# Kernel tuning notes

Hardware: AMD Instinct MI355X
Metric: run time of the kernel (lower is better)

## Reference

```python
import jax, jax.numpy as jnp
import numpy as np

MARGIN = 0.2


def _pairwise_euclidean(x):
    # [B, D] -> [B, B] euclidean distance matrix (safe sqrt: zero grad at d=0,
    # matching torch.cdist subgradient; diagonal is never used by the loss).
    sq = jnp.sum(x * x, axis=1)
    d2 = sq[:, None] + sq[None, :] - 2.0 * (x @ x.T)
    d2 = jnp.maximum(d2, 0.0)
    safe = jnp.where(d2 > 0, d2, 1.0)
    return jnp.where(d2 > 0, jnp.sqrt(safe), 0.0)


def setup_inputs() -> dict:
    key = jax.random.key(0)
    k1, k2 = jax.random.split(key)
    B, D = 256, 768
    return {
        "img_tokens": jax.random.normal(k1, (B, D), dtype=jnp.float32),
        "ehr_tokens": jax.random.normal(k2, (B, D), dtype=jnp.float32),
    }


def reference(img_tokens, ehr_tokens):
    B = img_tokens.shape[0]
    d_ehr = _pairwise_euclidean(ehr_tokens)  # [B, B]
    d_img = _pairwise_euclidean(img_tokens)  # [B, B]

    # Broadcast to [i, j, k] triplet grids.
    e_ij = d_ehr[:, :, None]
    e_ik = d_ehr[:, None, :]
    g_ij = d_img[:, :, None]
    g_ik = d_img[:, None, :]

    loss = jnp.where(
        e_ij < e_ik,
        jax.nn.relu(g_ij - g_ik + MARGIN),
        jnp.where(
            e_ik < e_ij,
            jax.nn.relu(g_ik - g_ij + MARGIN),
            jnp.abs(g_ij - g_ik),
        ),
    )  # [B, B, B]

    i = jnp.arange(B)[:, None, None]
    j = jnp.arange(B)[None, :, None]
    k = jnp.arange(B)[None, None, :]
    mask = (j < k) & (i != j) & (i != k)  # valid triplets: i!=j, i!=k, j<k

    num_triplets = B * (B - 1) * (B - 2) // 2  # B * C(B-1, 2)
    total = jnp.sum(jnp.where(mask, loss, 0.0))
    return total / num_triplets
```

## Files before the change

### kernel.cpp

```cpp
#include <hip/hip_runtime.h>
#include <math.h>

#define NB 256
#define ND 768
#define MARGIN_F 0.2f
#define NKC 16
#define KCF 48
#define PITCH 64

__global__ __launch_bounds__(256)
void dist_kernel(const float* __restrict__ Ximg,
                 const float* __restrict__ Xehr,
                 float* __restrict__ planes) {
    __shared__ float As[64 * PITCH];
    __shared__ float Bs[64 * PITCH];

    const int tid = threadIdx.x;
    const int bid = blockIdx.x;

    const int m    = bid >> 8;
    const int r    = bid & 255;
    const int tile = r >> 4;
    const int kc   = r & 15;
    const int ti   = tile >> 2;
    const int tj   = tile & 3;
    const float* __restrict__ X = m ? Xehr : Ximg;
    const int base_col = kc * KCF;

#pragma unroll
    for (int p = 0; p < 3; ++p) {
        const int idx = tid + (p << 8);
        const int row = idx / 12;
        const int c4  = idx - row * 12;
        const int sw  = (row >> 2) & 7;
        const float4 va = *(const float4*)(&X[(size_t)(ti * 64 + row) * ND + base_col + c4 * 4]);
        *(float4*)(&As[row * PITCH + ((c4 ^ sw) << 2)]) = va;
        const float4 vb = *(const float4*)(&X[(size_t)(tj * 64 + row) * ND + base_col + c4 * 4]);
        *(float4*)(&Bs[row * PITCH + ((c4 ^ sw) << 2)]) = vb;
    }
    __syncthreads();

    const int li = tid >> 4;
    const int lj = tid & 15;
    const int swa = li & 7;
    const int swb = lj & 7;

    float acc[4][4];
#pragma unroll
    for (int a = 0; a < 4; ++a)
#pragma unroll
        for (int b = 0; b < 4; ++b) acc[a][b] = 0.0f;

#pragma unroll 4
    for (int q = 0; q < 12; ++q) {
        float4 av[4], bv[4];
#pragma unroll
        for (int a = 0; a < 4; ++a)
            av[a] = *(const float4*)(&As[(4 * li + a) * PITCH + ((q ^ swa) << 2)]);
#pragma unroll
        for (int b = 0; b < 4; ++b)
            bv[b] = *(const float4*)(&Bs[(4 * lj + b) * PITCH + ((q ^ swb) << 2)]);
#pragma unroll
        for (int a = 0; a < 4; ++a)
#pragma unroll
            for (int b = 0; b < 4; ++b) {
                const float d0 = av[a].x - bv[b].x;
                const float d1 = av[a].y - bv[b].y;
                const float d2 = av[a].z - bv[b].z;
                const float d3 = av[a].w - bv[b].w;
                acc[a][b] += d0 * d0 + d1 * d1 + d2 * d2 + d3 * d3;
            }
    }

    float* P = planes + (((size_t)m * NKC + kc) << 16);
#pragma unroll
    for (int a = 0; a < 4; ++a) {
        const int gi = ti * 64 + 4 * li + a;
        float4 v;
        v.x = acc[a][0]; v.y = acc[a][1]; v.z = acc[a][2]; v.w = acc[a][3];
        *(float4*)(&P[(size_t)gi * NB + tj * 64 + 4 * lj]) = v;
    }
}

__global__ __launch_bounds__(512)
void triplet_kernel(const float* __restrict__ planes,
                    float* __restrict__ partials) {
    __shared__ float Es[NB], Gs[NB];
    __shared__ float pg[2][NB], pe[2][NB];
    __shared__ float wred[8];

    const int tid = threadIdx.x;
    const int i   = blockIdx.x;
    const int k   = tid & 255;
    const int h   = tid >> 8;

    float sg = 0.0f, se = 0.0f;
#pragma unroll
    for (int p = 0; p < 8; ++p) {
        const int pp = h * 8 + p;
        sg += planes[(((size_t)0 * NKC + pp) << 16) + (size_t)i * NB + k];
        se += planes[(((size_t)1 * NKC + pp) << 16) + (size_t)i * NB + k];
    }
    pg[h][k] = sg; pe[h][k] = se;
    __syncthreads();
    if (h == 0) {
        const float g2 = pg[0][k] + pg[1][k];
        const float e2 = pe[0][k] + pe[1][k];
        Gs[k] = (g2 > 0.0f) ? sqrtf(g2) : 0.0f;
        Es[k] = (e2 > 0.0f) ? sqrtf(e2) : 0.0f;
    }
    __syncthreads();

    const float ek = Es[k];
    const float gk = Gs[k];

    float local = 0.0f;
    const int j0 = h << 7;
#pragma unroll 4
    for (int jj = 0; jj < 128; ++jj) {
        const int j = j0 + jj;
        const float ej = Es[j];
        const float gj = Gs[j];
        const float diff = gj - gk;
        const float a = diff + MARGIN_F;
        const float b = MARGIN_F - diff;
        const float cc = fabsf(diff);
        const float sel = (ej < ek) ? a : ((ek < ej) ? b : cc);
        local += fmaxf(sel, 0.0f);
    }
    if (((i >> 7) == h) && (k != i)) local -= fmaxf(MARGIN_F - gk, 0.0f);
    if (k == i) local = 0.0f;

    for (int off = 32; off > 0; off >>= 1) local += __shfl_down(local, off, 64);
    const int wid = tid >> 6;
    const int lane = tid & 63;
    if (lane == 0) wred[wid] = local;
    __syncthreads();

    if (tid == 0) {
        float s = 0.0f;
#pragma unroll
        for (int w = 0; w < 8; ++w) s += wred[w];
        partials[i] = s;
    }
}

__global__ __launch_bounds__(256)
void reduce_kernel(const float* __restrict__ partials,
                   float* __restrict__ out) {
    const int tid = threadIdx.x;
    double v = (double)partials[tid];
    for (int off = 32; off > 0; off >>= 1) v += __shfl_down(v, off, 64);
    __shared__ double ds4[4];
    const int wid = tid >> 6;
    const int lane = tid & 63;
    if (lane == 0) ds4[wid] = v;
    __syncthreads();
    if (tid == 0) {
        const double total = ds4[0] + ds4[1] + ds4[2] + ds4[3];
        out[0] = (float)(total * 0.5 / 8290560.0);
    }
}

extern "C" void kernel_launch(void* const* d_in, const int* in_sizes, int n_in,
                              void* d_out, int out_size, void* d_ws, size_t ws_size,
                              hipStream_t stream) {
    const float* img = (const float*)d_in[0];
    const float* ehr = (const float*)d_in[1];
    float* out = (float*)d_out;

    float* planes   = (float*)d_ws;
    float* partials = planes + 2 * NKC * NB * NB;

    dist_kernel<<<dim3(512), 256, 0, stream>>>(img, ehr, planes);
    triplet_kernel<<<dim3(NB), 512, 0, stream>>>(planes, partials);
    reduce_kernel<<<dim3(1), 256, 0, stream>>>(partials, out);
}
```

Measured before the change: 23.78 us.

## Switch distance kernel to Gram formulation with row norms and simplify triplet loop

Pairwise squared distances are now formed as ||x_i||^2 + ||x_j||^2 - 2 x_i·x_j. Two extra blocks compute the row norms and the tiled kernel accumulates dot products in 64x128 tiles with 32 K-chunks of 24 columns. The triplet inner loop is reduced to one sign-select plus fmax, and the diagonal j==k and j==i terms are subtracted afterwards. The aim is to cut per-element ALU work in both kernels. The cost is twice as many partial planes written to and read from the workspace, plus the usual cancellation risk of the Gram form in fp32.

```diff
diff --git a/kernel.cpp b/kernel.cpp
--- a/kernel.cpp
+++ b/kernel.cpp
@@ -4,86 +4,105 @@
 #define NB 256
 #define ND 768
 #define MARGIN_F 0.2f
-#define NKC 16
-#define KCF 48
-#define PITCH 64
+#define NKC 32
+#define CHF 24
+#define PITCH 32
+
+__device__ __forceinline__ int swz(int row) { return ((row >> 3) ^ row) & 7; }
 
 __global__ __launch_bounds__(256)
 void dist_kernel(const float* __restrict__ Ximg,
                  const float* __restrict__ Xehr,
-                 float* __restrict__ planes) {
-    __shared__ float As[64 * PITCH];
-    __shared__ float Bs[64 * PITCH];
-
+                 float* __restrict__ planes,
+                 float* __restrict__ sqn) {
     const int tid = threadIdx.x;
     const int bid = blockIdx.x;
 
-    const int m    = bid >> 8;
-    const int r    = bid & 255;
-    const int tile = r >> 4;
-    const int kc   = r & 15;
-    const int ti   = tile >> 2;
-    const int tj   = tile & 3;
+    if (bid < 2) {
+        const int m = bid;
+        const float* __restrict__ X = m ? Xehr : Ximg;
+        const float4* xr = (const float4*)(X + (size_t)tid * ND);
+        float acc = 0.0f;
+#pragma unroll 8
+        for (int t = 0; t < ND / 4; ++t) {
+            const float4 v = xr[t];
+            acc += v.x * v.x + v.y * v.y + v.z * v.z + v.w * v.w;
+        }
+        sqn[m * NB + tid] = acc;
+        return;
+    }
+
+    __shared__ float S[(64 + 128) * PITCH];
+
+    const int cb   = bid - 2;
+    const int m    = cb >> 8;
+    const int r    = cb & 255;
+    const int tile = r >> 5;
+    const int kc   = r & 31;
+    const int ta   = tile >> 1;
+    const int tb   = tile & 1;
     const float* __restrict__ X = m ? Xehr : Ximg;
-    const int base_col = kc * KCF;
-
-#pragma unroll
-    for (int p = 0; p < 3; ++p) {
+    const int c0 = kc * CHF;
+
+    for (int p = 0; p < 5; ++p) {
         const int idx = tid + (p << 8);
-        const int row = idx / 12;
-        const int c4  = idx - row * 12;
-        const int sw  = (row >> 2) & 7;
-        const float4 va = *(const float4*)(&X[(size_t)(ti * 64 + row) * ND + base_col + c4 * 4]);
-        *(float4*)(&As[row * PITCH + ((c4 ^ sw) << 2)]) = va;
-        const float4 vb = *(const float4*)(&X[(size_t)(tj * 64 + row) * ND + base_col + c4 * 4]);
-        *(float4*)(&Bs[row * PITCH + ((c4 ^ sw) << 2)]) = vb;
+        if (idx < 1152) {
+            int row, c4, grow, base;
+            if (idx < 384) { row = idx / 6; c4 = idx - row * 6; grow = ta * 64 + row; base = 0; }
+            else { const int t2 = idx - 384; row = t2 / 6; c4 = t2 - row * 6; grow = tb * 128 + row; base = 64 * PITCH; }
+            const float4 v = *(const float4*)(&X[(size_t)grow * ND + c0 + c4 * 4]);
+            *(float4*)(&S[base + row * PITCH + ((c4 ^ swz(row)) << 2)]) = v;
+        }
     }
     __syncthreads();
 
     const int li = tid >> 4;
     const int lj = tid & 15;
-    const int swa = li & 7;
-    const int swb = lj & 7;
-
-    float acc[4][4];
+    int sA[4], sB[8];
+#pragma unroll
+    for (int a = 0; a < 4; ++a) sA[a] = swz(4 * li + a);
+#pragma unroll
+    for (int b = 0; b < 8; ++b) sB[b] = swz(8 * lj + b);
+
+    float acc[4][8];
 #pragma unroll
     for (int a = 0; a < 4; ++a)
 #pragma unroll
-        for (int b = 0; b < 4; ++b) acc[a][b] = 0.0f;
-
-#pragma unroll 4
-    for (int q = 0; q < 12; ++q) {
-        float4 av[4], bv[4];
+        for (int b = 0; b < 8; ++b) acc[a][b] = 0.0f;
+
+#pragma unroll
+    for (int q = 0; q < 6; ++q) {
+        float4 av[4], bv[8];
 #pragma unroll
         for (int a = 0; a < 4; ++a)
-            av[a] = *(const float4*)(&As[(4 * li + a) * PITCH + ((q ^ swa) << 2)]);
-#pragma unroll
-        for (int b = 0; b < 4; ++b)
-            bv[b] = *(const float4*)(&Bs[(4 * lj + b) * PITCH + ((q ^ swb) << 2)]);
+            av[a] = *(const float4*)(&S[(4 * li + a) * PITCH + ((q ^ sA[a]) << 2)]);
+#pragma unroll
+        for (int b = 0; b < 8; ++b)
+            bv[b] = *(const float4*)(&S[64 * PITCH + (8 * lj + b) * PITCH + ((q ^ sB[b]) << 2)]);
 #pragma unroll
         for (int a = 0; a < 4; ++a)
 #pragma unroll
-            for (int b = 0; b < 4; ++b) {
-                const float d0 = av[a].x - bv[b].x;
-                const float d1 = av[a].y - bv[b].y;
-                const float d2 = av[a].z - bv[b].z;
-                const float d3 = av[a].w - bv[b].w;
-                acc[a][b] += d0 * d0 + d1 * d1 + d2 * d2 + d3 * d3;
-            }
+            for (int b = 0; b < 8; ++b)
+                acc[a][b] += av[a].x * bv[b].x + av[a].y * bv[b].y +
+                             av[a].z * bv[b].z + av[a].w * bv[b].w;
     }
 
     float* P = planes + (((size_t)m * NKC + kc) << 16);
 #pragma unroll
     for (int a = 0; a < 4; ++a) {
-        const int gi = ti * 64 + 4 * li + a;
-        float4 v;
-        v.x = acc[a][0]; v.y = acc[a][1]; v.z = acc[a][2]; v.w = acc[a][3];
-        *(float4*)(&P[(size_t)gi * NB + tj * 64 + 4 * lj]) = v;
+        const int gi = ta * 64 + 4 * li + a;
+        const int cb0 = tb * 128 + 8 * lj;
+        float4 v0, v1;
+        v0.x = acc[a][0]; v0.y = acc[a][1]; v0.z = acc[a][2]; v0.w = acc[a][3];
+        v1.x = acc[a][4]; v1.y = acc[a][5]; v1.z = acc[a][6]; v1.w = acc[a][7];
+        *(float4*)(&P[(size_t)gi * NB + cb0])     = v0;
+        *(float4*)(&P[(size_t)gi * NB + cb0 + 4]) = v1;
     }
 }
 
 __global__ __launch_bounds__(512)
 void triplet_kernel(const float* __restrict__ planes,
+                    const float* __restrict__ sqn,
                     float* __restrict__ partials) {
     __shared__ float Es[NB], Gs[NB];
     __shared__ float pg[2][NB], pe[2][NB];
@@ -96,18 +115,20 @@
 
     float sg = 0.0f, se = 0.0f;
 #pragma unroll
-    for (int p = 0; p < 8; ++p) {
-        const int pp = h * 8 + p;
-        sg += planes[(((size_t)0 * NKC + pp) << 16) + (size_t)i * NB + k];
-        se += planes[(((size_t)1 * NKC + pp) << 16) + (size_t)i * NB + k];
+    for (int p = 0; p < 16; ++p) {
+        const int pp = h * 16 + p;
+        sg += planes[((size_t)pp << 16) + (size_t)i * NB + k];
+        se += planes[((size_t)(NKC + pp) << 16) + (size_t)i * NB + k];
     }
     pg[h][k] = sg; pe[h][k] = se;
     __syncthreads();
     if (h == 0) {
-        const float g2 = pg[0][k] + pg[1][k];
-        const float e2 = pe[0][k] + pe[1][k];
-        Gs[k] = (g2 > 0.0f) ? sqrtf(g2) : 0.0f;
-        Es[k] = (e2 > 0.0f) ? sqrtf(e2) : 0.0f;
+        const float dg = pg[0][k] + pg[1][k];
+        const float de = pe[0][k] + pe[1][k];
+        const float d2g = sqn[i] + sqn[k] - 2.0f * dg;
+        const float d2e = sqn[NB + i] + sqn[NB + k] - 2.0f * de;
+        Gs[k] = (d2g > 0.0f) ? sqrtf(d2g) : 0.0f;
+        Es[k] = (d2e > 0.0f) ? sqrtf(d2e) : 0.0f;
     }
     __syncthreads();
 
@@ -116,19 +137,19 @@
 
     float local = 0.0f;
     const int j0 = h << 7;
-#pragma unroll 4
+#pragma unroll 8
     for (int jj = 0; jj < 128; ++jj) {
         const int j = j0 + jj;
-        const float ej = Es[j];
-        const float gj = Gs[j];
-        const float diff = gj - gk;
-        const float a = diff + MARGIN_F;
-        const float b = MARGIN_F - diff;
-        const float cc = fabsf(diff);
-        const float sel = (ej < ek) ? a : ((ek < ej) ? b : cc);
-        local += fmaxf(sel, 0.0f);
-    }
-    if (((i >> 7) == h) && (k != i)) local -= fmaxf(MARGIN_F - gk, 0.0f);
+        const float diff = Gs[j] - gk;
+        const float s = (Es[j] < ek) ? diff : -diff;
+        local += fmaxf(MARGIN_F + s, 0.0f);
+    }
+    if (((k >> 7) == h) && (k != i)) local -= MARGIN_F;
+    if (((i >> 7) == h) && (k != i)) {
+        const float diff = Gs[i] - gk;
+        const float s = (Es[i] < ek) ? diff : -diff;
+        local -= fmaxf(MARGIN_F + s, 0.0f);
+    }
     if (k == i) local = 0.0f;
 
     for (int off = 32; off > 0; off >>= 1) local += __shfl_down(local, off, 64);
@@ -170,9 +191,10 @@
     float* out = (float*)d_out;
 
     float* planes   = (float*)d_ws;
-    float* partials = planes + 2 * NKC * NB * NB;
-
-    dist_kernel<<<dim3(512), 256, 0, stream>>>(img, ehr, planes);
-    triplet_kernel<<<dim3(NB), 512, 0, stream>>>(planes, partials);
+    float* sqn      = planes + 2 * NKC * NB * NB;
+    float* partials = sqn + 2 * NB;
+
+    dist_kernel<<<dim3(514), 256, 0, stream>>>(img, ehr, planes, sqn);
+    triplet_kernel<<<dim3(NB), 512, 0, stream>>>(planes, sqn, partials);
     reduce_kernel<<<dim3(1), 256, 0, stream>>>(partials, out);
 }
```

New measurement: 39.43 us. 65.8% more time.
